# Kernel optimization log

Hardware: AMD Instinct MI355X
Metric: run time of the kernel (lower is better)

Reference implementation:

```python
import jax, jax.numpy as jnp
import numpy as np

B, L, E, H = 4, 1024, 2048, 16
DH = E // H
SCALE_BASE = 512.0


def _rotate_every_two(x):
    x1 = x[..., ::2]
    x2 = x[..., 1::2]
    return jnp.stack([-x2, x1], axis=-1).reshape(x.shape)


def _xpos(x, downscale):
    # x: [BH, L, Dh]; non-incremental path => offset = 0
    length = x.shape[1]
    head_dim = x.shape[-1]
    min_pos = -(length // 2)
    positions = jnp.arange(min_pos, length + min_pos, dtype=jnp.float32)  # [L]
    base = (jnp.arange(0, head_dim, 2, dtype=jnp.float32) + 0.4 * head_dim) / (1.4 * head_dim)  # [Dh/2]
    scale = base[None, :] ** (positions[:, None] / SCALE_BASE)  # [L, Dh/2]
    # fixed_pos_embedding over `scale` (seq_len=L, dim=Dh/2), positions 0..L-1
    dim = head_dim // 2
    inv_freq = 1.0 / (10000.0 ** (jnp.arange(0, dim, dtype=jnp.float32) / dim))
    sinusoid = jnp.arange(length, dtype=jnp.float32)[:, None] * inv_freq[None, :]
    sin, cos = jnp.sin(sinusoid), jnp.cos(sinusoid)
    if downscale:
        scale = 1.0 / scale
    sin_s = jnp.repeat(sin * scale, 2, axis=-1)  # duplicate_interleave -> [L, Dh]
    cos_s = jnp.repeat(cos * scale, 2, axis=-1)
    return x * cos_s + _rotate_every_two(x) * sin_s


def setup_inputs() -> dict:
    key = jax.random.key(0)
    ks = jax.random.split(key, 6)
    w_std = 1.0 / np.sqrt(E)
    query = jax.random.normal(ks[0], (B, L, E), dtype=jnp.float32)
    Wq = jax.random.normal(ks[1], (E, E), dtype=jnp.float32) * w_std
    Wk = jax.random.normal(ks[2], (E, E), dtype=jnp.float32) * w_std
    Wv = jax.random.normal(ks[3], (E, E), dtype=jnp.float32) * w_std
    Wo = jax.random.normal(ks[4], (E, E), dtype=jnp.float32) * w_std
    bq = jnp.zeros((E,), jnp.float32)
    bk = jnp.zeros((E,), jnp.float32)
    bv = jnp.zeros((E,), jnp.float32)
    bo = jnp.zeros((E,), jnp.float32)
    # causal additive mask [L, L]: 0 on/below diag, large negative above
    attn_mask = jnp.where(jnp.triu(jnp.ones((L, L), bool), k=1), -1e9, 0.0).astype(jnp.float32)
    rel_pos = jax.random.normal(ks[5], (B * H, L, L), dtype=jnp.float32) * 0.02
    return {"query": query, "Wq": Wq, "bq": bq, "Wk": Wk, "bk": bk, "Wv": Wv,
            "bv": bv, "Wo": Wo, "bo": bo, "attn_mask": attn_mask, "rel_pos": rel_pos}


def reference(query, Wq, bq, Wk, bk, Wv, bv, Wo, bo, attn_mask, rel_pos):
    scaling = DH ** -0.5
    q = (query @ Wq.T + bq) * scaling
    k = query @ Wk.T + bk
    v = query @ Wv.T + bv

    def split(t):  # [B, L, E] -> [B*H, L, Dh]
        return t.reshape(B, L, H, DH).transpose(0, 2, 1, 3).reshape(B * H, L, DH)

    q, k, v = split(q), split(k), split(v)
    k = _xpos(k, downscale=True)
    q = _xpos(q, downscale=False)

    w = jnp.einsum('btd,bsd->bts', q, k)          # [B*H, L, L]
    w = jnp.nan_to_num(w) + attn_mask[None]
    w = w + rel_pos
    w = jax.nn.softmax(w.astype(jnp.float32), axis=-1).astype(w.dtype)
    attn = jnp.einsum('bts,bsd->btd', w, v)       # [B*H, L, Dh]
    attn = attn.reshape(B, H, L, DH).transpose(0, 2, 1, 3).reshape(B, L, E)
    out = attn @ Wo.T + bo
    attn_weights = w.reshape(B, H, L, L).transpose(1, 0, 2, 3)  # [H, B, L, L]
    return out, attn_weights
```

## Files before the change

### kernel.cpp

```cpp
#include <hip/hip_runtime.h>
#include <math.h>

#define BB 4
#define LL 1024
#define EE 2048
#define HH 16
#define DHD 128
#define NTOK 4096
#define NBH 64
#define OUT0_ELEMS 8388608

typedef __attribute__((ext_vector_type(8))) short short8;
typedef __attribute__((ext_vector_type(4))) float f32x4;
typedef __attribute__((ext_vector_type(4))) unsigned short ushort4v;
typedef __attribute__((ext_vector_type(8))) unsigned short ushort8v;

__device__ __forceinline__ unsigned short f2bf(float x) {
    union { float f; unsigned int u; } v; v.f = x;
    unsigned int r = v.u + 0x7FFFu + ((v.u >> 16) & 1u);
    return (unsigned short)(r >> 16);
}
__device__ __forceinline__ float bf2f(unsigned short h) {
    union { unsigned int u; float f; } v; v.u = ((unsigned int)h) << 16;
    return v.f;
}

__device__ __forceinline__ void gload16(const void* g, void* l) {
    __builtin_amdgcn_global_load_lds((const __attribute__((address_space(1))) void*)g,
                                     (__attribute__((address_space(3))) void*)l,
                                     16, 0, 0);
}

__global__ __launch_bounds__(256)
void cvt_all_k(const float* __restrict__ X, const float* __restrict__ Wq,
               const float* __restrict__ Wk, const float* __restrict__ Wv,
               const float* __restrict__ Wo, unsigned short* __restrict__ Xbf,
               unsigned short* __restrict__ Wqkvb, unsigned short* __restrict__ Wob) {
    size_t g = (size_t)(blockIdx.x * 256 + threadIdx.x) * 8;
    if (g >= 25165824u) return;
    const float* src;
    unsigned short* dst;
    if (g < 8388608u) {
        src = X + g; dst = Xbf + g;
    } else {
        size_t rr = g - 8388608u;
        int wi = (int)(rr >> 22);
        size_t o = rr & 4194303u;
        src = (wi == 0 ? Wq : wi == 1 ? Wk : wi == 2 ? Wv : Wo) + o;
        dst = (wi < 3 ? Wqkvb + ((size_t)wi << 22) : Wob) + o;
    }
    float4 a = *(const float4*)(src);
    float4 b = *(const float4*)(src + 4);
    ushort4v u, w;
    u.x = f2bf(a.x); u.y = f2bf(a.y); u.z = f2bf(a.z); u.w = f2bf(a.w);
    w.x = f2bf(b.x); w.y = f2bf(b.y); w.z = f2bf(b.z); w.w = f2bf(b.w);
    *(ushort4v*)(dst) = u;
    *(ushort4v*)(dst + 4) = w;
}

__global__ __launch_bounds__(64) void xpos_table_k(float4* __restrict__ tab) {
    int t = blockIdx.x;
    int j = threadIdx.x;
    float pos = (float)(t - 512);
    float base = (2.0f * (float)j + 51.2f) * (1.0f / 179.2f);
    float sc = powf(base, pos * (1.0f / 512.0f));
    float inv_freq = powf(10000.0f, -(float)j * (1.0f / 64.0f));
    float ang = (float)t * inv_freq;
    float s = sinf(ang);
    float c = cosf(ang);
    tab[(t << 6) | j] = make_float4(c * sc, s * sc, c / sc, s / sc);
}

template <int MODE>
__global__ __launch_bounds__(512, 2)
void mm8_k(const unsigned short* __restrict__ Abf, const unsigned short* __restrict__ Bw,
           const float* __restrict__ bq, const float* __restrict__ bk,
           const float* __restrict__ bv, unsigned short* __restrict__ qb,
           unsigned short* __restrict__ kb, unsigned short* __restrict__ vt,
           const float4* __restrict__ tab, float* __restrict__ Cout,
           float scaling) {
    __shared__ alignas(16) char smem[131072];

    const int tid = threadIdx.x;
    const int lane = tid & 63;
    const int wid = tid >> 6;
    const int wr = wid >> 2;
    const int wcn = wid & 3;
    const int fr = lane & 15, fq = lane >> 4;

    int bx, by;
    if constexpr (MODE == 0) {
        const int flat = blockIdx.y * 24 + blockIdx.x;
        const int xcd = flat & 7, rmp = flat >> 3;
        bx = xcd * 3 + rmp % 3;
        by = rmp / 3;
    } else {
        const int flat = blockIdx.y * 8 + blockIdx.x;
        bx = flat & 7;
        by = flat >> 3;
    }
    const int m0 = by * 256, n0 = bx * 256;

    auto stageA = [&](int T, int half) {
        char* dst = smem + ((T & 1) << 16) + (half << 14);
        const unsigned short* src = Abf + (size_t)(m0 + half * 128) * 2048 + T * 64;
#pragma unroll
        for (int j = 0; j < 2; ++j) {
            int o = (j * 512 + tid) * 16;
            int r = o >> 7;
            int cs = ((o & 127) >> 4) ^ (r & 7);
            gload16(src + (size_t)r * 2048 + cs * 8, dst + o);
        }
    };
    auto stageB = [&](int T, int half) {
        char* dst = smem + ((T & 1) << 16) + 32768 + (half << 14);
        const unsigned short* src = Bw + (size_t)(n0 + half * 128) * 2048 + T * 64;
#pragma unroll
        for (int j = 0; j < 2; ++j) {
            int o = (j * 512 + tid) * 16;
            int r = o >> 7;
            int cs = ((o & 127) >> 4) ^ (r & 7);
            gload16(src + (size_t)r * 2048 + cs * 8, dst + o);
        }
    };
    auto rdA = [&](int buf, int mi, int ks) -> short8 {
        int rl = mi * 16 + fr;
        const char* base = smem + (buf << 16) + (wr << 14);
        return *(const short8*)(base + rl * 128 + ((ks * 4 + fq) ^ (rl & 7)) * 16);
    };
    auto rdB = [&](int buf, int ni, int ks) -> short8 {
        int rb = ((wcn & 1) << 6) + ni * 16 + fr;
        const char* base = smem + (buf << 16) + 32768 + ((wcn >> 1) << 14);
        return *(const short8*)(base + rb * 128 + ((ks * 4 + fq) ^ (rb & 7)) * 16);
    };

    f32x4 acc[8][4];
#pragma unroll
    for (int i = 0; i < 8; ++i)
#pragma unroll
        for (int j = 0; j < 4; ++j) acc[i][j] = (f32x4){0.f, 0.f, 0.f, 0.f};

    stageA(0, 0); stageA(0, 1); stageB(0, 0); stageB(0, 1);
    stageB(1, 0); stageB(1, 1);

    for (int T = 0; T < 32; ++T) {
        const int buf = T & 1;
        if (T < 31) asm volatile("s_waitcnt vmcnt(4)" ::: "memory");
        else        asm volatile("s_waitcnt vmcnt(0)" ::: "memory");
        __builtin_amdgcn_s_barrier();

        short8 af[2][4], bf[2][4];

#pragma unroll
        for (int mi = 0; mi < 4; ++mi) { af[0][mi] = rdA(buf, mi, 0); af[1][mi] = rdA(buf, mi, 1); }
#pragma unroll
        for (int ni = 0; ni < 2; ++ni) { bf[0][ni] = rdB(buf, ni, 0); bf[1][ni] = rdB(buf, ni, 1); }
        if (T < 31) stageA(T + 1, 0);
        __builtin_amdgcn_s_barrier();
        __builtin_amdgcn_s_setprio(1);
#pragma unroll
        for (int mi = 0; mi < 4; ++mi)
#pragma unroll
            for (int ni = 0; ni < 2; ++ni) {
                acc[mi][ni] = __builtin_amdgcn_mfma_f32_16x16x32_bf16(af[0][mi], bf[0][ni], acc[mi][ni], 0, 0, 0);
                acc[mi][ni] = __builtin_amdgcn_mfma_f32_16x16x32_bf16(af[1][mi], bf[1][ni], acc[mi][ni], 0, 0, 0);
            }
        __builtin_amdgcn_s_setprio(0);
        __builtin_amdgcn_s_barrier();

#pragma unroll
        for (int ni = 2; ni < 4; ++ni) { bf[0][ni] = rdB(buf, ni, 0); bf[1][ni] = rdB(buf, ni, 1); }
        if (T < 31) stageA(T + 1, 1);
        __builtin_amdgcn_s_barrier();
        __builtin_amdgcn_s_setprio(1);
#pragma unroll
        for (int mi = 0; mi < 4; ++mi)
#pragma unroll
            for (int ni = 2; ni < 4; ++ni) {
                acc[mi][ni] = __builtin_amdgcn_mfma_f32_16x16x32_bf16(af[0][mi], bf[0][ni], acc[mi][ni], 0, 0, 0);
                acc[mi][ni] = __builtin_amdgcn_mfma_f32_16x16x32_bf16(af[1][mi], bf[1][ni], acc[mi][ni], 0, 0, 0);
            }
        __builtin_amdgcn_s_setprio(0);
        __builtin_amdgcn_s_barrier();

#pragma unroll
        for (int mi = 0; mi < 4; ++mi) { af[0][mi] = rdA(buf, mi + 4, 0); af[1][mi] = rdA(buf, mi + 4, 1); }
        if (T < 30) stageB(T + 2, 0);
        __builtin_amdgcn_s_barrier();
        __builtin_amdgcn_s_setprio(1);
#pragma unroll
        for (int mi = 0; mi < 4; ++mi)
#pragma unroll
            for (int ni = 2; ni < 4; ++ni) {
                acc[mi + 4][ni] = __builtin_amdgcn_mfma_f32_16x16x32_bf16(af[0][mi], bf[0][ni], acc[mi + 4][ni], 0, 0, 0);
                acc[mi + 4][ni] = __builtin_amdgcn_mfma_f32_16x16x32_bf16(af[1][mi], bf[1][ni], acc[mi + 4][ni], 0, 0, 0);
            }
        __builtin_amdgcn_s_setprio(0);
        __builtin_amdgcn_s_barrier();

        if (T < 30) stageB(T + 2, 1);
        __builtin_amdgcn_s_barrier();
        __builtin_amdgcn_s_setprio(1);
#pragma unroll
        for (int mi = 0; mi < 4; ++mi)
#pragma unroll
            for (int ni = 0; ni < 2; ++ni) {
                acc[mi + 4][ni] = __builtin_amdgcn_mfma_f32_16x16x32_bf16(af[0][mi], bf[0][ni], acc[mi + 4][ni], 0, 0, 0);
                acc[mi + 4][ni] = __builtin_amdgcn_mfma_f32_16x16x32_bf16(af[1][mi], bf[1][ni], acc[mi + 4][ni], 0, 0, 0);
            }
        __builtin_amdgcn_s_setprio(0);
        __builtin_amdgcn_s_barrier();
    }

    if constexpr (MODE == 1) {
        const float* bias = bq;
#pragma unroll
        for (int mi = 0; mi < 8; ++mi)
#pragma unroll
            for (int ni = 0; ni < 4; ++ni)
#pragma unroll
                for (int rg = 0; rg < 4; ++rg) {
                    int m = m0 + wr * 128 + mi * 16 + fq * 4 + rg;
                    int n = n0 + wcn * 64 + ni * 16 + fr;
                    Cout[(size_t)m * EE + n] = acc[mi][ni][rg] + bias[n];
                }
        return;
    } else {
        const int w = n0 >> 11;
        const float* bsel = (w == 0) ? bq : (w == 1) ? bk : bv;
        const float alpha = (w == 0) ? scaling : 1.0f;
        const int hbase = (n0 & 2047) >> 7;
        const int b_ = m0 >> 10;
        const int m0r = m0 & 1023;
        float* slab = (float*)smem;

        unsigned short* qk = (w == 0) ? qb : kb;
#pragma unroll
        for (int sl = 0; sl < 8; ++sl) {
            if (wr == (sl >> 2)) {
#pragma unroll
                for (int mi2 = 0; mi2 < 2; ++mi2) {
                    int mi = ((sl & 3) << 1) + mi2;
#pragma unroll
                    for (int ni = 0; ni < 4; ++ni) {
                        int scol = wcn * 64 + ni * 16 + fr;
                        float bias = bsel[(n0 & 2047) + scol];
#pragma unroll
                        for (int rg = 0; rg < 4; ++rg) {
                            int srow = (mi2 << 4) + fq * 4 + rg;
                            slab[srow * 260 + scol] = alpha * (acc[mi][ni][rg] + bias);
                        }
                    }
                }
            }
            __syncthreads();

            if (w < 2) {
                int sr = tid >> 4, cg = tid & 15;
                int t = m0r + (sl << 5) + sr;
                int h = hbase + (cg >> 3);
                int d0 = (cg & 7) << 4;
                const float* SR = slab + sr * 260 + cg * 16;
                ushort8v h0, h1;
#pragma unroll
                for (int p = 0; p < 4; ++p) {
                    float x = SR[2 * p], y = SR[2 * p + 1];
                    float4 tb = tab[(t << 6) | ((d0 >> 1) + p)];
                    float c = (w == 0) ? tb.x : tb.z;
                    float s = (w == 0) ? tb.y : tb.w;
                    h0[2 * p]     = f2bf(x * c - y * s);
                    h0[2 * p + 1] = f2bf(y * c + x * s);
                }
#pragma unroll
                for (int p = 0; p < 4; ++p) {
                    float x = SR[8 + 2 * p], y = SR[8 + 2 * p + 1];
                    float4 tb = tab[(t << 6) | ((d0 >> 1) + 4 + p)];
                    float c = (w == 0) ? tb.x : tb.z;
                    float s = (w == 0) ? tb.y : tb.w;
                    h1[2 * p]     = f2bf(x * c - y * s);
                    h1[2 * p + 1] = f2bf(y * c + x * s);
                }
                unsigned short* DR = qk + (((size_t)(b_ * HH + h)) << 17) + ((size_t)t << 7) + d0;
                *(ushort8v*)(DR) = h0;
                *(ushort8v*)(DR + 8) = h1;
            } else {
                int vcol = tid >> 1, th = tid & 1;
                int h = hbase + (vcol >> 7), d = vcol & 127;
                ushort8v h0, h1;
#pragma unroll
                for (int p = 0; p < 8; ++p)
                    h0[p] = f2bf(slab[(th * 16 + p) * 260 + vcol]);
#pragma unroll
                for (int p = 0; p < 8; ++p)
                    h1[p] = f2bf(slab[(th * 16 + 8 + p) * 260 + vcol]);
                unsigned short* DR = vt + (((size_t)((b_ * HH + h) * 128 + d)) << 10)
                                     + m0r + (sl << 5);
                DR += th * 16;
                *(ushort8v*)(DR) = h0;
                *(ushort8v*)(DR + 8) = h1;
            }
            __syncthreads();
        }
    }
}

__global__ __launch_bounds__(256)
void scores_k(const unsigned short* __restrict__ qb, const unsigned short* __restrict__ kb,
              const float* __restrict__ rel, unsigned short* __restrict__ ebuf,
              float* __restrict__ psum) {
    __shared__ alignas(16) char smem[16384];
    unsigned short* lA = (unsigned short*)smem;
    unsigned short* lB = (unsigned short*)(smem + 8192);
    float* slab = (float*)smem;

    const int tid = threadIdx.x;
    const int lane = tid & 63, wave = tid >> 6;
    const int wr = wave >> 1, wc = wave & 1;
    const int fr = lane & 15, fq = lane >> 4;

    const int flat = blockIdx.y * 36 + blockIdx.x;
    const int xcd = flat & 7, rmp = flat >> 3;
    int idx = rmp % 36;
    const int bh = (rmp / 36) * 8 + xcd;

    int tt = (int)((sqrtf(8.f * (float)idx + 1.f) - 1.f) * 0.5f);
    while ((tt + 1) * (tt + 2) / 2 <= idx) ++tt;
    while (tt * (tt + 1) / 2 > idx) --tt;
    const int ss = idx - tt * (tt + 1) / 2;
    const int t0 = tt << 7, s0 = ss << 7;

    const unsigned short* Q = qb + ((size_t)bh << 17);
    const unsigned short* K = kb + ((size_t)bh << 17);

    f32x4 acc[4][4];
#pragma unroll
    for (int i = 0; i < 4; ++i)
#pragma unroll
        for (int j = 0; j < 4; ++j) acc[i][j] = (f32x4){0.f, 0.f, 0.f, 0.f};

    for (int k0 = 0; k0 < 128; k0 += 32) {
#pragma unroll
        for (int i = 0; i < 2; ++i) {
            int c = i * 256 + tid;
            int r = c >> 2, kc = c & 3;
            gload16(Q + (size_t)(t0 + r) * 128 + k0 + kc * 8, &lA[c * 8]);
        }
#pragma unroll
        for (int i = 0; i < 2; ++i) {
            int c = i * 256 + tid;
            int r = c >> 2, kc = c & 3;
            gload16(K + (size_t)(s0 + r) * 128 + k0 + kc * 8, &lB[c * 8]);
        }
        __syncthreads();

        short8 afr[4], bfr[4];
#pragma unroll
        for (int mi = 0; mi < 4; ++mi)
            afr[mi] = *(const short8*)&lA[(wr * 64 + mi * 16 + fr) * 32 + fq * 8];
#pragma unroll
        for (int ni = 0; ni < 4; ++ni)
            bfr[ni] = *(const short8*)&lB[(wc * 64 + ni * 16 + fr) * 32 + fq * 8];
#pragma unroll
        for (int mi = 0; mi < 4; ++mi)
#pragma unroll
            for (int ni = 0; ni < 4; ++ni)
                acc[mi][ni] = __builtin_amdgcn_mfma_f32_16x16x32_bf16(
                    afr[mi], bfr[ni], acc[mi][ni], 0, 0, 0);
        __syncthreads();
    }

    unsigned short* EO = ebuf + ((size_t)bh << 20);
    const float* RLb = rel + ((size_t)bh << 20);
#pragma unroll
    for (int sl = 0; sl < 4; ++sl) {
        if (wr == (sl >> 1)) {
#pragma unroll
            for (int mi2 = 0; mi2 < 2; ++mi2) {
                int mi = ((sl & 1) << 1) + mi2;
#pragma unroll
                for (int ni = 0; ni < 4; ++ni)
#pragma unroll
                    for (int r = 0; r < 4; ++r) {
                        int srow = (mi2 << 4) + (fq << 2) + r;
                        int col = (wc << 6) + (ni << 4) + fr;
                        slab[srow * 128 + (col ^ (((srow >> 2) & 3) << 4))] = acc[mi][ni][r];
                    }
            }
        }
        __syncthreads();
        {
            int srow = tid >> 3;
            int tg = t0 + (sl << 5) + srow;
            const float* RL = RLb + ((size_t)tg << 10) + s0;
            unsigned short* ER = EO + ((size_t)tg << 10) + s0;
            float rsum = 0.f;
#pragma unroll
            for (int c = 0; c < 4; ++c) {
                int col = ((tid & 7) << 2) + (c << 5);
                float4 sv = *(const float4*)&slab[srow * 128 + (col ^ (((srow >> 2) & 3) << 4))];
                float4 rl = *(const float4*)(RL + col);
                float4 e;
                e.x = (s0 + col     <= tg) ? __expf(sv.x + rl.x - 15.f) : 0.f;
                e.y = (s0 + col + 1 <= tg) ? __expf(sv.y + rl.y - 15.f) : 0.f;
                e.z = (s0 + col + 2 <= tg) ? __expf(sv.z + rl.z - 15.f) : 0.f;
                e.w = (s0 + col + 3 <= tg) ? __expf(sv.w + rl.w - 15.f) : 0.f;
                ushort4v h;
                h.x = f2bf(e.x); h.y = f2bf(e.y); h.z = f2bf(e.z); h.w = f2bf(e.w);
                *(ushort4v*)(ER + col) = h;
                rsum += e.x + e.y + e.z + e.w;
            }
            rsum += __shfl_xor(rsum, 1);
            rsum += __shfl_xor(rsum, 2);
            rsum += __shfl_xor(rsum, 4);
            if ((tid & 7) == 0)
                psum[((((size_t)bh << 10) + tg) << 3) + ss] = rsum;
        }
        __syncthreads();
    }
}

__global__ __launch_bounds__(256)
void pvw_k(const unsigned short* __restrict__ ebuf, const unsigned short* __restrict__ vt,
           const float* __restrict__ psum, float* __restrict__ attnP,
           unsigned short* __restrict__ am) {
    __shared__ alignas(16) unsigned short lE[64 * 64];
    __shared__ alignas(16) unsigned short lV[128 * 64];
    __shared__ float lInvF[64];

    const int tid = threadIdx.x;
    const int lane = tid & 63, wave = tid >> 6;
    const int wr = wave >> 1, wc = wave & 1;
    const int fr = lane & 15, fq = lane >> 4;
    const int strip = 15 - blockIdx.y;
    const int t0 = strip << 6;
    const int bh = blockIdx.x;
    const int hh = bh & 15, bb = bh >> 4;
    const int n_s = (t0 >> 6) + 1;

    const unsigned short* EB = ebuf + ((size_t)bh << 20) + ((size_t)t0 << 10);
    const unsigned short* Vb = vt + ((size_t)bh << 17);
    float* PO = attnP + (((size_t)(hh * BB + bb)) << 20) + ((size_t)t0 << 10);

    if (tid < 64) {
        const float* p = psum + ((((size_t)bh << 10) + t0 + tid) << 3);
        const int tt = t0 >> 7;
        float s = 0.f;
#pragma unroll
        for (int j = 0; j < 8; ++j) s += (j <= tt) ? p[j] : 0.f;
        lInvF[tid] = 1.f / s;
    }
    __syncthreads();

    f32x4 acc[2][4];
#pragma unroll
    for (int i = 0; i < 2; ++i)
#pragma unroll
        for (int j = 0; j < 4; ++j) acc[i][j] = (f32x4){0.f, 0.f, 0.f, 0.f};

    for (int j = 0; j < n_s; ++j) {
        int s0 = j << 6;
#pragma unroll
        for (int i = 0; i < 2; ++i) {
            int o = (i * 256 + tid) * 16;
            int r = o >> 7;
            int cb = (o & 127) ^ ((r & 7) << 4);
            gload16(EB + (size_t)r * 1024 + s0 + (cb >> 1), (char*)lE + o);
        }
#pragma unroll
        for (int i = 0; i < 4; ++i) {
            int o = (i * 256 + tid) * 16;
            int r = o >> 7;
            int cb = (o & 127) ^ ((r & 7) << 4);
            gload16(Vb + (size_t)r * 1024 + s0 + (cb >> 1), (char*)lV + o);
        }
        __syncthreads();

        {
            int row = tid >> 2, col0 = (tid & 3) << 4;
            float inv = lInvF[row];
            float* PR = PO + (size_t)row * 1024 + s0 + col0;
#pragma unroll
            for (int cc = 0; cc < 2; ++cc) {
                int cbyte = ((col0 + cc * 8) * 2) ^ ((row & 7) << 4);
                ushort8v ev = *(const ushort8v*)((const char*)lE + row * 128 + cbyte);
                float4 p0, p1;
                p0.x = bf2f(ev[0]) * inv; p0.y = bf2f(ev[1]) * inv;
                p0.z = bf2f(ev[2]) * inv; p0.w = bf2f(ev[3]) * inv;
                p1.x = bf2f(ev[4]) * inv; p1.y = bf2f(ev[5]) * inv;
                p1.z = bf2f(ev[6]) * inv; p1.w = bf2f(ev[7]) * inv;
                *(float4*)(PR + cc * 8) = p0;
                *(float4*)(PR + cc * 8 + 4) = p1;
            }
        }

#pragma unroll
        for (int ks = 0; ks < 2; ++ks) {
            short8 pf[2], vf[4];
#pragma unroll
            for (int mi = 0; mi < 2; ++mi) {
                int row = wr * 32 + mi * 16 + fr;
                int cb = (ks * 64 + fq * 16) ^ ((row & 7) << 4);
                pf[mi] = *(const short8*)((const char*)lE + row * 128 + cb);
            }
#pragma unroll
            for (int ni = 0; ni < 4; ++ni) {
                int row = wc * 64 + ni * 16 + fr;
                int cb = (ks * 64 + fq * 16) ^ ((row & 7) << 4);
                vf[ni] = *(const short8*)((const char*)lV + row * 128 + cb);
            }
#pragma unroll
            for (int mi = 0; mi < 2; ++mi)
#pragma unroll
                for (int ni = 0; ni < 4; ++ni)
                    acc[mi][ni] = __builtin_amdgcn_mfma_f32_16x16x32_bf16(
                        pf[mi], vf[ni], acc[mi][ni], 0, 0, 0);
        }
        __syncthreads();
    }

    {
        int row = tid >> 2;
        float4 z = make_float4(0.f, 0.f, 0.f, 0.f);
        for (int c = (n_s << 6) + ((tid & 3) << 2); c < 1024; c += 16)
            *(float4*)(PO + (size_t)row * 1024 + c) = z;
    }

#pragma unroll
    for (int mi = 0; mi < 2; ++mi)
#pragma unroll
        for (int ni = 0; ni < 4; ++ni)
#pragma unroll
            for (int r = 0; r < 4; ++r) {
                int tl = wr * 32 + mi * 16 + fq * 4 + r;
                int d = wc * 64 + ni * 16 + fr;
                float o = acc[mi][ni][r] * lInvF[tl];
                am[(((size_t)(bb * 1024 + t0 + tl)) << 11) + hh * 128 + d] = f2bf(o);
            }
}

extern "C" void kernel_launch(void* const* d_in, const int* in_sizes, int n_in,
                              void* d_out, int out_size, void* d_ws, size_t ws_size,
                              hipStream_t stream) {
    const float* query = (const float*)d_in[0];
    const float* Wq    = (const float*)d_in[1];
    const float* bq    = (const float*)d_in[2];
    const float* Wk    = (const float*)d_in[3];
    const float* bk    = (const float*)d_in[4];
    const float* Wv    = (const float*)d_in[5];
    const float* bv    = (const float*)d_in[6];
    const float* Wo    = (const float*)d_in[7];
    const float* bo    = (const float*)d_in[8];
    const float* rel   = (const float*)d_in[10];

    float* out    = (float*)d_out;
    float* attn_w = out + OUT0_ELEMS;

    char* w = (char*)d_ws;
    unsigned short* Xbf   = (unsigned short*)(w);
    unsigned short* Wqkvb = (unsigned short*)(w + (16 << 20));
    unsigned short* Wob   = (unsigned short*)(w + (40 << 20));
    unsigned short* qb    = (unsigned short*)(w + (48 << 20));
    unsigned short* kb    = (unsigned short*)(w + (64 << 20));
    unsigned short* vt    = (unsigned short*)(w + (80 << 20));
    unsigned short* am    = (unsigned short*)(w + (96 << 20));
    float4* tab           = (float4*)(w + (112 << 20));
    float* psum           = (float*)(w + (113u << 20));
    unsigned short* ebuf  = (unsigned short*)(w + (128u << 20));

    const float scaling = 0.08838834764831845f;

    xpos_table_k<<<LL, 64, 0, stream>>>(tab);

    cvt_all_k<<<12288, 256, 0, stream>>>(query, Wq, Wk, Wv, Wo, Xbf, Wqkvb, Wob);

    dim3 gqkv(24, 16);
    mm8_k<0><<<gqkv, 512, 0, stream>>>(Xbf, Wqkvb, bq, bk, bv, qb, kb, vt, tab,
                                       nullptr, scaling);

    dim3 gsc(36, NBH);
    scores_k<<<gsc, 256, 0, stream>>>(qb, kb, rel, ebuf, psum);

    dim3 gpv(NBH, 16);
    pvw_k<<<gpv, 256, 0, stream>>>(ebuf, vt, psum, attn_w, am);

    dim3 gout(8, 16);
    mm8_k<1><<<gout, 512, 0, stream>>>(am, Wob, bo, nullptr, nullptr, nullptr,
                                       nullptr, nullptr, tab, out, 1.0f);
}
```

Measured before the change: 456.6 us.

## Shrink GEMM M-tile to 128 rows and drop XCD-aware block remap

Halves the M tile of the shared GEMM kernel from 256 to 128 rows. This cuts LDS from 128KB to 96KB, halves the accumulator registers per thread, and doubles the grid for the QKV and output projections, aiming at better occupancy and wave count on the CUs. The XCD-aware block swizzle is removed in favour of plain blockIdx mapping, and an extra __syncthreads is added before the epilogue reuses smem. The trade-off is lower arithmetic intensity per tile, more redundant B-tile loads, and worse L2 locality without the remap.

After: 426.7 us. -6.6%, faster.

```diff
diff --git a/kernel.cpp b/kernel.cpp
--- a/kernel.cpp
+++ b/kernel.cpp
@@ -79,7 +79,7 @@
            unsigned short* __restrict__ kb, unsigned short* __restrict__ vt,
            const float4* __restrict__ tab, float* __restrict__ Cout,
            float scaling) {
-    __shared__ alignas(16) char smem[131072];
+    __shared__ alignas(16) char smem[98304];
 
     const int tid = threadIdx.x;
     const int lane = tid & 63;
@@ -88,22 +88,11 @@
     const int wcn = wid & 3;
     const int fr = lane & 15, fq = lane >> 4;
 
-    int bx, by;
-    if constexpr (MODE == 0) {
-        const int flat = blockIdx.y * 24 + blockIdx.x;
-        const int xcd = flat & 7, rmp = flat >> 3;
-        bx = xcd * 3 + rmp % 3;
-        by = rmp / 3;
-    } else {
-        const int flat = blockIdx.y * 8 + blockIdx.x;
-        bx = flat & 7;
-        by = flat >> 3;
-    }
-    const int m0 = by * 256, n0 = bx * 256;
-
-    auto stageA = [&](int T, int half) {
-        char* dst = smem + ((T & 1) << 16) + (half << 14);
-        const unsigned short* src = Abf + (size_t)(m0 + half * 128) * 2048 + T * 64;
+    const int m0 = blockIdx.y * 128, n0 = blockIdx.x * 256;
+
+    auto stageA = [&](int T) {
+        char* dst = smem + ((T & 1) << 14);
+        const unsigned short* src = Abf + (size_t)m0 * 2048 + T * 64;
 #pragma unroll
         for (int j = 0; j < 2; ++j) {
             int o = (j * 512 + tid) * 16;
@@ -113,7 +102,7 @@
         }
     };
     auto stageB = [&](int T, int half) {
-        char* dst = smem + ((T & 1) << 16) + 32768 + (half << 14);
+        char* dst = smem + 32768 + ((T & 1) << 15) + (half << 14);
         const unsigned short* src = Bw + (size_t)(n0 + half * 128) * 2048 + T * 64;
 #pragma unroll
         for (int j = 0; j < 2; ++j) {
@@ -124,24 +113,24 @@
         }
     };
     auto rdA = [&](int buf, int mi, int ks) -> short8 {
-        int rl = mi * 16 + fr;
-        const char* base = smem + (buf << 16) + (wr << 14);
+        int rl = (wr << 6) + mi * 16 + fr;
+        const char* base = smem + (buf << 14);
         return *(const short8*)(base + rl * 128 + ((ks * 4 + fq) ^ (rl & 7)) * 16);
     };
     auto rdB = [&](int buf, int ni, int ks) -> short8 {
-        int rb = ((wcn & 1) << 6) + ni * 16 + fr;
-        const char* base = smem + (buf << 16) + 32768 + ((wcn >> 1) << 14);
-        return *(const short8*)(base + rb * 128 + ((ks * 4 + fq) ^ (rb & 7)) * 16);
+        int rb = wcn * 64 + ni * 16 + fr;
+        const char* base = smem + 32768 + (buf << 15) + ((rb >> 7) << 14);
+        int rh = rb & 127;
+        return *(const short8*)(base + rh * 128 + ((ks * 4 + fq) ^ (rh & 7)) * 16);
     };
 
-    f32x4 acc[8][4];
-#pragma unroll
-    for (int i = 0; i < 8; ++i)
+    f32x4 acc[4][4];
+#pragma unroll
+    for (int i = 0; i < 4; ++i)
 #pragma unroll
         for (int j = 0; j < 4; ++j) acc[i][j] = (f32x4){0.f, 0.f, 0.f, 0.f};
 
-    stageA(0, 0); stageA(0, 1); stageB(0, 0); stageB(0, 1);
-    stageB(1, 0); stageB(1, 1);
+    stageA(0); stageB(0, 0); stageB(0, 1); stageB(1, 0); stageB(1, 1);
 
     for (int T = 0; T < 32; ++T) {
         const int buf = T & 1;
@@ -149,51 +138,50 @@
         else        asm volatile("s_waitcnt vmcnt(0)" ::: "memory");
         __builtin_amdgcn_s_barrier();
 
-        short8 af[2][4], bf[2][4];
-
-#pragma unroll
-        for (int mi = 0; mi < 4; ++mi) { af[0][mi] = rdA(buf, mi, 0); af[1][mi] = rdA(buf, mi, 1); }
-#pragma unroll
-        for (int ni = 0; ni < 2; ++ni) { bf[0][ni] = rdB(buf, ni, 0); bf[1][ni] = rdB(buf, ni, 1); }
-        if (T < 31) stageA(T + 1, 0);
+        short8 a0[2][2], a1[2][2], b0[2][2], b1[2][2];
+
+#pragma unroll
+        for (int mi = 0; mi < 2; ++mi) { a0[mi][0] = rdA(buf, mi, 0); a0[mi][1] = rdA(buf, mi, 1); }
+#pragma unroll
+        for (int ni = 0; ni < 2; ++ni) { b0[ni][0] = rdB(buf, ni, 0); b0[ni][1] = rdB(buf, ni, 1); }
+        if (T < 31) stageA(T + 1);
         __builtin_amdgcn_s_barrier();
         __builtin_amdgcn_s_setprio(1);
 #pragma unroll
-        for (int mi = 0; mi < 4; ++mi)
+        for (int mi = 0; mi < 2; ++mi)
 #pragma unroll
             for (int ni = 0; ni < 2; ++ni) {
-                acc[mi][ni] = __builtin_amdgcn_mfma_f32_16x16x32_bf16(af[0][mi], bf[0][ni], acc[mi][ni], 0, 0, 0);
-                acc[mi][ni] = __builtin_amdgcn_mfma_f32_16x16x32_bf16(af[1][mi], bf[1][ni], acc[mi][ni], 0, 0, 0);
+                acc[mi][ni] = __builtin_amdgcn_mfma_f32_16x16x32_bf16(a0[mi][0], b0[ni][0], acc[mi][ni], 0, 0, 0);
+                acc[mi][ni] = __builtin_amdgcn_mfma_f32_16x16x32_bf16(a0[mi][1], b0[ni][1], acc[mi][ni], 0, 0, 0);
             }
         __builtin_amdgcn_s_setprio(0);
         __builtin_amdgcn_s_barrier();
 
 #pragma unroll
-        for (int ni = 2; ni < 4; ++ni) { bf[0][ni] = rdB(buf, ni, 0); bf[1][ni] = rdB(buf, ni, 1); }
-        if (T < 31) stageA(T + 1, 1);
+        for (int ni = 0; ni < 2; ++ni) { b1[ni][0] = rdB(buf, ni + 2, 0); b1[ni][1] = rdB(buf, ni + 2, 1); }
         __builtin_amdgcn_s_barrier();
         __builtin_amdgcn_s_setprio(1);
 #pragma unroll
-        for (int mi = 0; mi < 4; ++mi)
-#pragma unroll
-            for (int ni = 2; ni < 4; ++ni) {
-                acc[mi][ni] = __builtin_amdgcn_mfma_f32_16x16x32_bf16(af[0][mi], bf[0][ni], acc[mi][ni], 0, 0, 0);
-                acc[mi][ni] = __builtin_amdgcn_mfma_f32_16x16x32_bf16(af[1][mi], bf[1][ni], acc[mi][ni], 0, 0, 0);
+        for (int mi = 0; mi < 2; ++mi)
+#pragma unroll
+            for (int ni = 0; ni < 2; ++ni) {
+                acc[mi][ni + 2] = __builtin_amdgcn_mfma_f32_16x16x32_bf16(a0[mi][0], b1[ni][0], acc[mi][ni + 2], 0, 0, 0);
+                acc[mi][ni + 2] = __builtin_amdgcn_mfma_f32_16x16x32_bf16(a0[mi][1], b1[ni][1], acc[mi][ni + 2], 0, 0, 0);
             }
         __builtin_amdgcn_s_setprio(0);
         __builtin_amdgcn_s_barrier();
 
 #pragma unroll
-        for (int mi = 0; mi < 4; ++mi) { af[0][mi] = rdA(buf, mi + 4, 0); af[1][mi] = rdA(buf, mi + 4, 1); }
+        for (int mi = 0; mi < 2; ++mi) { a1[mi][0] = rdA(buf, mi + 2, 0); a1[mi][1] = rdA(buf, mi + 2, 1); }
         if (T < 30) stageB(T + 2, 0);
         __builtin_amdgcn_s_barrier();
         __builtin_amdgcn_s_setprio(1);
 #pragma unroll
-        for (int mi = 0; mi < 4; ++mi)
-#pragma unroll
-            for (int ni = 2; ni < 4; ++ni) {
-                acc[mi + 4][ni] = __builtin_amdgcn_mfma_f32_16x16x32_bf16(af[0][mi], bf[0][ni], acc[mi + 4][ni], 0, 0, 0);
-                acc[mi + 4][ni] = __builtin_amdgcn_mfma_f32_16x16x32_bf16(af[1][mi], bf[1][ni], acc[mi + 4][ni], 0, 0, 0);
+        for (int mi = 0; mi < 2; ++mi)
+#pragma unroll
+            for (int ni = 0; ni < 2; ++ni) {
+                acc[mi + 2][ni] = __builtin_amdgcn_mfma_f32_16x16x32_bf16(a1[mi][0], b0[ni][0], acc[mi + 2][ni], 0, 0, 0);
+                acc[mi + 2][ni] = __builtin_amdgcn_mfma_f32_16x16x32_bf16(a1[mi][1], b0[ni][1], acc[mi + 2][ni], 0, 0, 0);
             }
         __builtin_amdgcn_s_setprio(0);
         __builtin_amdgcn_s_barrier();
@@ -202,11 +190,11 @@
         __builtin_amdgcn_s_barrier();
         __builtin_amdgcn_s_setprio(1);
 #pragma unroll
-        for (int mi = 0; mi < 4; ++mi)
+        for (int mi = 0; mi < 2; ++mi)
 #pragma unroll
             for (int ni = 0; ni < 2; ++ni) {
-                acc[mi + 4][ni] = __builtin_amdgcn_mfma_f32_16x16x32_bf16(af[0][mi], bf[0][ni], acc[mi + 4][ni], 0, 0, 0);
-                acc[mi + 4][ni] = __builtin_amdgcn_mfma_f32_16x16x32_bf16(af[1][mi], bf[1][ni], acc[mi + 4][ni], 0, 0, 0);
+                acc[mi + 2][ni + 2] = __builtin_amdgcn_mfma_f32_16x16x32_bf16(a1[mi][0], b1[ni][0], acc[mi + 2][ni + 2], 0, 0, 0);
+                acc[mi + 2][ni + 2] = __builtin_amdgcn_mfma_f32_16x16x32_bf16(a1[mi][1], b1[ni][1], acc[mi + 2][ni + 2], 0, 0, 0);
             }
         __builtin_amdgcn_s_setprio(0);
         __builtin_amdgcn_s_barrier();
@@ -215,12 +203,12 @@
     if constexpr (MODE == 1) {
         const float* bias = bq;
 #pragma unroll
-        for (int mi = 0; mi < 8; ++mi)
+        for (int mi = 0; mi < 4; ++mi)
 #pragma unroll
             for (int ni = 0; ni < 4; ++ni)
 #pragma unroll
                 for (int rg = 0; rg < 4; ++rg) {
-                    int m = m0 + wr * 128 + mi * 16 + fq * 4 + rg;
+                    int m = m0 + wr * 64 + mi * 16 + fq * 4 + rg;
                     int n = n0 + wcn * 64 + ni * 16 + fr;
                     Cout[(size_t)m * EE + n] = acc[mi][ni][rg] + bias[n];
                 }
@@ -235,12 +223,13 @@
         float* slab = (float*)smem;
 
         unsigned short* qk = (w == 0) ? qb : kb;
-#pragma unroll
-        for (int sl = 0; sl < 8; ++sl) {
-            if (wr == (sl >> 2)) {
+        __syncthreads();
+#pragma unroll
+        for (int sl = 0; sl < 4; ++sl) {
+            if (wr == (sl >> 1)) {
 #pragma unroll
                 for (int mi2 = 0; mi2 < 2; ++mi2) {
-                    int mi = ((sl & 3) << 1) + mi2;
+                    int mi = ((sl & 1) << 1) + mi2;
 #pragma unroll
                     for (int ni = 0; ni < 4; ++ni) {
                         int scol = wcn * 64 + ni * 16 + fr;
@@ -294,8 +283,7 @@
                 for (int p = 0; p < 8; ++p)
                     h1[p] = f2bf(slab[(th * 16 + 8 + p) * 260 + vcol]);
                 unsigned short* DR = vt + (((size_t)((b_ * HH + h) * 128 + d)) << 10)
-                                     + m0r + (sl << 5);
-                DR += th * 16;
+                                     + m0r + (sl << 5) + th * 16;
                 *(ushort8v*)(DR) = h0;
                 *(ushort8v*)(DR + 8) = h1;
             }
@@ -573,7 +561,7 @@
 
     cvt_all_k<<<12288, 256, 0, stream>>>(query, Wq, Wk, Wv, Wo, Xbf, Wqkvb, Wob);
 
-    dim3 gqkv(24, 16);
+    dim3 gqkv(24, 32);
     mm8_k<0><<<gqkv, 512, 0, stream>>>(Xbf, Wqkvb, bq, bk, bv, qb, kb, vt, tab,
                                        nullptr, scaling);
 
@@ -583,7 +571,7 @@
     dim3 gpv(NBH, 16);
     pvw_k<<<gpv, 256, 0, stream>>>(ebuf, vt, psum, attn_w, am);
 
-    dim3 gout(8, 16);
+    dim3 gout(8, 32);
     mm8_k<1><<<gout, 512, 0, stream>>>(am, Wob, bo, nullptr, nullptr, nullptr,
                                        nullptr, nullptr, tab, out, 1.0f);
 }
```
